# Performance work log

Measured on AMD Instinct MI355X. Metric: run time of the kernel, lower is better.

The kernel has to match this reference:

```python
import jax, jax.numpy as jnp
import numpy as np

H = 64       # HIDDEN_DIM
NH = 2       # attention heads
HD = H // NH # head dim = 32
M = 8        # MEMORY_SLOTS
V = 64       # VOCAB_SIZE


def layer_norm(x, g, b):
    m = x.mean(-1, keepdims=True)
    v = ((x - m) ** 2).mean(-1, keepdims=True)
    return (x - m) / jnp.sqrt(v + 1e-5) * g + b


def mha(x, wi, bi, wo, bo):
    # torch nn.MultiheadAttention, batch_first, self-attention, avg head weights
    B, L, _ = x.shape
    qkv = x @ wi.T + bi                      # (B,L,3H)
    q, k, v = jnp.split(qkv, 3, axis=-1)
    q = q.reshape(B, L, NH, HD)
    k = k.reshape(B, L, NH, HD)
    v = v.reshape(B, L, NH, HD)
    s = jnp.einsum('bqhd,bkhd->bhqk', q, k) / jnp.sqrt(jnp.float32(HD))
    w = jax.nn.softmax(s, axis=-1)           # (B,NH,L,L)
    o = jnp.einsum('bhqk,bkhd->bqhd', w, v).reshape(B, L, H)
    return o @ wo.T + bo, w.mean(axis=1)     # averaged over heads


def ffn(x, w1, b1, w2, b2):
    return jax.nn.relu(x @ w1.T + b1) @ w2.T + b2


def setup_inputs() -> dict:
    key = jax.random.key(0)
    ks = iter(jax.random.split(key, 48))
    p = lambda shape: jax.random.normal(next(ks), shape, jnp.float32) * 0.02
    B, L = 16, 2048
    inp = {
        'seq': jax.random.randint(next(ks), (B, L), 0, V, jnp.int64 if jax.config.jax_enable_x64 else jnp.int32),
        'query': jax.random.randint(next(ks), (B,), 0, V, jnp.int32),
        'target': jax.random.randint(next(ks), (B,), 0, V, jnp.int32),
        'embed': p((V, H)),
        'a1_wi': p((3 * H, H)), 'a1_bi': p((3 * H,)), 'a1_wo': p((H, H)), 'a1_bo': p((H,)),
        'ff1_w1': p((2 * H, H)), 'ff1_b1': p((2 * H,)), 'ff1_w2': p((H, 2 * H)), 'ff1_b2': p((H,)),
        'ln1a_g': jnp.ones((H,)), 'ln1a_b': jnp.zeros((H,)),
        'ln1b_g': jnp.ones((H,)), 'ln1b_b': jnp.zeros((H,)),
        'a2_wi': p((3 * H, H)), 'a2_bi': p((3 * H,)), 'a2_wo': p((H, H)), 'a2_bo': p((H,)),
        'ff2_w1': p((2 * H, H)), 'ff2_b1': p((2 * H,)), 'ff2_w2': p((H, 2 * H)), 'ff2_b2': p((H,)),
        'ln2a_g': jnp.ones((H,)), 'ln2a_b': jnp.zeros((H,)),
        'ln2b_g': jnp.ones((H,)), 'ln2b_b': jnp.zeros((H,)),
        'rq_w': p((H, H)), 'rq_b': p((H,)),
        'ro_w': p((V, H)), 'ro_b': p((V,)),
        'qemb': p((V, H)),
    }
    return inp


def reference(seq, query, target, embed,
              a1_wi, a1_bi, a1_wo, a1_bo, ff1_w1, ff1_b1, ff1_w2, ff1_b2,
              ln1a_g, ln1a_b, ln1b_g, ln1b_b,
              a2_wi, a2_bi, a2_wo, a2_bo, ff2_w1, ff2_b1, ff2_w2, ff2_b2,
              ln2a_g, ln2a_b, ln2b_g, ln2b_b,
              rq_w, rq_b, ro_w, ro_b, qemb):
    # encoder
    h = embed[seq]                                        # (B,L,H)
    a1, _ = mha(h, a1_wi, a1_bi, a1_wo, a1_bo)
    h = layer_norm(h + a1, ln1a_g, ln1a_b)
    h = layer_norm(h + ffn(h, ff1_w1, ff1_b1, ff1_w2, ff1_b2), ln1b_g, ln1b_b)
    a2, attn_w = mha(h, a2_wi, a2_bi, a2_wo, a2_bo)       # attn_w: (B,L,L)
    h = layer_norm(h + a2, ln2a_g, ln2a_b)
    h = layer_norm(h + ffn(h, ff2_w1, ff2_b1, ff2_w2, ff2_b2), ln2b_g, ln2b_b)

    # slot selection (write_mode='attention'): per-key importance, top-k
    importance = attn_w.mean(axis=1)                      # (B,L)
    _, topk = jax.lax.top_k(importance, M)                # (B,M)
    mem = jnp.take_along_axis(h, topk[:, :, None], axis=1)  # (B,M,H)

    # memory reader
    q_h = qemb[query]                                     # (B,H)
    q = q_h @ rq_w.T + rq_b                               # (B,H)
    scores = (q[:, None, :] * mem).sum(-1) / jnp.sqrt(jnp.float32(H))  # (B,M)
    weights = jax.nn.softmax(scores, axis=-1)[:, :, None]
    read = (weights * mem).sum(1)                         # (B,H)
    logits = read @ ro_w.T + ro_b                         # (B,V)

    logp = jax.nn.log_softmax(logits, axis=-1)
    loss = -jnp.mean(logp[jnp.arange(logits.shape[0]), target])
    return loss, attn_w
```

## Files before the change

kernel.cpp:

```cpp
#include <hip/hip_runtime.h>
#include <hip/hip_bf16.h>


typedef unsigned short u16;
#define LQ 2048
#define BBATCH 16
#define QKB 262144

typedef __attribute__((ext_vector_type(8))) short bf16x8;
typedef __attribute__((ext_vector_type(4))) float f32x4;

__device__ __forceinline__ float bfu2f(u16 x){ return __uint_as_float(((unsigned)x) << 16); }
__device__ __forceinline__ u16 f2bu(float f){ return __bfloat16_as_ushort(__float2bfloat16(f)); }

__device__ __forceinline__ unsigned cvtpk(float lo, float hi){
  unsigned r;
  asm("v_cvt_pk_bf16_f32 %0, %1, %2" : "=v"(r) : "v"(lo), "v"(hi));
  return r;
}

__device__ __forceinline__ const u16* qk_rowp(const u16* qk_r15, const u16* qk_ws,
                                              int bz, int row){
  const u16* base = (bz < 15) ? (qk_r15 + (size_t)bz*QKB) : qk_ws;
  return base + (size_t)row*128;
}
__device__ __forceinline__ u16* qk_rowp_w(u16* qk_r15, u16* qk_ws, int bz, int row){
  u16* base = (bz < 15) ? (qk_r15 + (size_t)bz*QKB) : qk_ws;
  return base + (size_t)row*128;
}

__global__ __launch_bounds__(256) void k_embed(const int* __restrict__ seq,
                                               const float* __restrict__ emb,
                                               u16* __restrict__ h,
                                               float* __restrict__ imp0,
                                               float* __restrict__ out0){
  int i = blockIdx.x*256 + threadIdx.x;
  if (i < 32768) imp0[i] = 0.f;
  if (i == 0) out0[0] = 0.f;
  int tok = i >> 6, d = i & 63;
  int v = seq[tok] & 63;
  h[i] = f2bu(emb[(v << 6) + d]);
}

template<int MODE>
__global__ __launch_bounds__(256) void k_qkv(const u16* __restrict__ X,
                                             const float* __restrict__ W,
                                             const float* __restrict__ bias,
                                             u16* __restrict__ dqk0,
                                             u16* __restrict__ dqk_r15,
                                             u16* __restrict__ dqk_ws,
                                             u16* __restrict__ vg){
  __shared__ u16 WL[192*64];
  __shared__ unsigned YL32[64*97];
  __shared__ float BS[192];
  const int t = threadIdx.x;
  for (int e=t; e<12288; e+=256){
    int m = e>>6, k = e&63;
    WL[m*64 + (k ^ ((m&7)<<3))] = f2bu(W[e]);
  }
  if (t < 192) BS[t] = bias[t];
  __syncthreads();
  const int lane = t & 63, wv = t >> 6;
  const int n = lane & 15, gq = lane >> 4;
  const int tok0 = blockIdx.x*64;
  const int tl = wv*16 + n;
  bf16x8 xf0 = *(const bf16x8*)(X + (size_t)(tok0+tl)*64 + gq*8);
  bf16x8 xf1 = *(const bf16x8*)(X + (size_t)(tok0+tl)*64 + 32 + gq*8);
  const float qs = 0.17677669529663688f;
  #pragma unroll
  for (int ct=0; ct<12; ct++){
    f32x4 c;
    #pragma unroll
    for (int r=0;r<4;r++) c[r] = BS[ct*16 + gq*4 + r];
    bf16x8 wf0 = *(const bf16x8*)(WL + (ct*16+n)*64 + ((gq*8) ^ ((n&7)<<3)));
    bf16x8 wf1 = *(const bf16x8*)(WL + (ct*16+n)*64 + ((32+gq*8) ^ ((n&7)<<3)));
    c = __builtin_amdgcn_mfma_f32_16x16x32_bf16(wf0, xf0, c, 0, 0, 0);
    c = __builtin_amdgcn_mfma_f32_16x16x32_bf16(wf1, xf1, c, 0, 0, 0);
    if (ct < 4){ c[0]*=qs; c[1]*=qs; c[2]*=qs; c[3]*=qs; }
    YL32[tl*97 + ct*8 + gq*2]     = cvtpk(c[0], c[1]);
    YL32[tl*97 + ct*8 + gq*2 + 1] = cvtpk(c[2], c[3]);
  }
  __syncthreads();
  const int b = tok0 >> 11, rbase = tok0 & 2047;
  #pragma unroll
  for (int i=0;i<16;i++){
    int idx = i*256 + t;
    int rl = idx>>6, cc = idx&63;
    u16* row = (MODE==0) ? (dqk0 + (size_t)(tok0+rl)*128)
                         : qk_rowp_w(dqk_r15, dqk_ws, b, rbase+rl);
    ((unsigned*)row)[cc] = YL32[rl*97 + cc];
  }
  #pragma unroll
  for (int i=0;i<4;i++){
    int gid = i*256 + t;
    int grp = gid>>6, d = gid&63;
    int j0 = rbase + grp*4;
    unsigned lohi[2];
    #pragma unroll
    for (int p=0;p<2;p++){
      unsigned w0 = YL32[(grp*4 + 2*p)*97 + 64 + (d>>1)];
      unsigned w1 = YL32[(grp*4 + 2*p + 1)*97 + 64 + (d>>1)];
      u16 a  = (d&1) ? (u16)(w0>>16) : (u16)(w0 & 0xffffu);
      u16 bb = (d&1) ? (u16)(w1>>16) : (u16)(w1 & 0xffffu);
      lohi[p] = (unsigned)a | ((unsigned)bb << 16);
    }
    size_t A = ((size_t)((b*64 + (j0>>5))*4 + ((j0>>2)&3))*64 + d)*8 + ((j0>>4)&1)*4;
    *(uint2*)(vg + A) = make_uint2(lohi[0], lohi[1]);
  }
}

template<int MODE>
__global__ __launch_bounds__(256) void k_attn_ln(const u16* __restrict__ PQK,
    const u16* __restrict__ QKWS, const u16* __restrict__ VG,
    const float* __restrict__ wo, const float* __restrict__ bo,
    const float* __restrict__ g, const float* __restrict__ be,
    u16* __restrict__ h, float* __restrict__ lout){
  __shared__ float R[4096];
  __shared__ float ST[32*68];
  __shared__ float DN[2][32];
  __shared__ float CB[192];
  const int lin = blockIdx.x;
  const int nid = (lin & 7)*128 + (lin >> 3);
  const int qt = nid & 63, bz = nid >> 6;
  const int t = threadIdx.x;
  const int lane = t & 63, wv = t >> 6;
  const int n = lane & 15, gq = lane >> 4;
  const f32x4 FZ = {0.f, 0.f, 0.f, 0.f};

  for (int e=t; e<2048; e+=256) R[e] = 0.f;
  if (t < 64) DN[t>>5][t&31] = 0.f;
  __syncthreads();

  bf16x8 qf[2][2];
  #pragma unroll
  for (int qa=0; qa<2; qa++){
    const u16* qrow = (MODE==0) ? (PQK + (size_t)(bz*LQ + qt*32 + qa*16 + n)*128)
                                : qk_rowp(PQK, QKWS, bz, qt*32 + qa*16 + n);
    qf[qa][0] = *(const bf16x8*)(qrow + gq*8);
    qf[qa][1] = *(const bf16x8*)(qrow + 32 + gq*8);
  }
  f32x4 o[2][2][2];
  #pragma unroll
  for (int qa=0; qa<2; qa++)
    #pragma unroll
    for (int hh=0; hh<2; hh++)
      #pragma unroll
      for (int db=0; db<2; db++) o[qa][hh][db] = FZ;
  float dacc[2][2] = {{0.f,0.f},{0.f,0.f}};

  #pragma unroll 1
  for (int kt=wv*8; kt<wv*8+8; kt++){
    #pragma unroll
    for (int hh=0; hh<2; hh++){
      bf16x8 kf[4];
      #pragma unroll
      for (int jb=0; jb<4; jb++){
        const u16* kr = (MODE==0) ? (PQK + (size_t)(bz*LQ + kt*64 + jb*16 + n)*128)
                                  : qk_rowp(PQK, QKWS, bz, kt*64 + jb*16 + n);
        kf[jb] = *(const bf16x8*)(kr + 64 + hh*32 + gq*8);
      }
      unsigned pk[2][4][2];
      #pragma unroll
      for (int qa=0; qa<2; qa++){
        f32x4 ev[4];
        #pragma unroll
        for (int jb=0; jb<4; jb++)
          ev[jb] = __builtin_amdgcn_mfma_f32_16x16x32_bf16(kf[jb], qf[qa][hh], FZ, 0, 0, 0);
        float ds = 0.f;
        #pragma unroll
        for (int jb=0; jb<4; jb++){
          float e0 = __expf(ev[jb][0]), e1 = __expf(ev[jb][1]);
          float e2 = __expf(ev[jb][2]), e3 = __expf(ev[jb][3]);
          ds += (e0+e1) + (e2+e3);
          pk[qa][jb][0] = cvtpk(e0, e1);
          pk[qa][jb][1] = cvtpk(e2, e3);
        }
        dacc[qa][hh] += ds;
      }
      #pragma unroll
      for (int kb=0; kb<2; kb++){
        union { unsigned u[4]; bf16x8 v; } af[2];
        #pragma unroll
        for (int qa=0; qa<2; qa++){
          af[qa].u[0] = pk[qa][2*kb][0];   af[qa].u[1] = pk[qa][2*kb][1];
          af[qa].u[2] = pk[qa][2*kb+1][0]; af[qa].u[3] = pk[qa][2*kb+1][1];
        }
        #pragma unroll
        for (int db=0; db<2; db++){
          const int d = hh*32 + db*16 + n;
          const bf16x8 vf = *(const bf16x8*)(VG +
              ((size_t)((bz*64 + kt*2 + kb)*4 + gq)*64 + d)*8);
          #pragma unroll
          for (int qa=0; qa<2; qa++)
            o[qa][hh][db] = __builtin_amdgcn_mfma_f32_16x16x32_bf16(af[qa].v, vf, o[qa][hh][db], 0, 0, 0);
        }
      }
    }
  }
  #pragma unroll
  for (int qa=0; qa<2; qa++)
    #pragma unroll
    for (int hh=0; hh<2; hh++){
      float s = dacc[qa][hh];
      s += __shfl_xor(s, 16);
      s += __shfl_xor(s, 32);
      if (gq == 0) atomicAdd(&DN[hh][qa*16 + n], s);
    }
  #pragma unroll
  for (int qa=0; qa<2; qa++)
    #pragma unroll
    for (int hh=0; hh<2; hh++)
      #pragma unroll
      for (int db=0; db<2; db++)
        #pragma unroll
        for (int r=0; r<4; r++)
          atomicAdd(&R[(qa*16 + gq*4 + r)*64 + hh*32 + db*16 + n], o[qa][hh][db][r]);
  __syncthreads();
  if (lout && t < 64)
    lout[(size_t)(bz*2 + (t>>5))*LQ + qt*32 + (t&31)] = DN[t>>5][t&31];
  for (int e=t; e<2048; e+=256){
    int q = e >> 6, d = e & 63;
    ST[q*68 + d] = R[e] / DN[d>>5][q];
  }
  __syncthreads();
  for (int e2=t; e2<4096; e2+=256){ int k=e2>>6, mo=e2&63; R[e2] = wo[mo*64+k]; }
  if (t < 64)       CB[t] = bo[t];
  else if (t < 128) CB[t] = g[t-64];
  else if (t < 192) CB[t] = be[t-128];
  __syncthreads();
  for (int r=0; r<8; r++){
    int tl = wv*8 + r;
    size_t gtok = (size_t)(bz*LQ + qt*32 + tl);
    float acc = CB[lane];
    for (int k=0; k<64; k++) acc += ST[tl*68 + k] * R[k*64 + lane];
    float rr = acc + bfu2f(h[gtok*64 + lane]);
    float s = rr;
    #pragma unroll
    for (int ofs=32; ofs; ofs>>=1) s += __shfl_xor(s, ofs);
    float mean = s * (1.f/64.f);
    float dv = rr - mean;
    float vs = dv*dv;
    #pragma unroll
    for (int ofs=32; ofs; ofs>>=1) vs += __shfl_xor(vs, ofs);
    float rstd = 1.f/sqrtf(vs*(1.f/64.f) + 1e-5f);
    h[gtok*64 + lane] = f2bu(dv*rstd*CB[64+lane] + CB[128+lane]);
  }
}

__global__ __launch_bounds__(256) void k_ffn(u16* __restrict__ h,
    const float* __restrict__ w1, const float* __restrict__ b1,
    const float* __restrict__ w2, const float* __restrict__ b2,
    const float* __restrict__ g, const float* __restrict__ be){
  __shared__ u16 W1L[128*64];
  __shared__ u16 W2L[64*192];
  __shared__ u16 YL[64*64];
  __shared__ float B1[128], B2F[64], G[64], Bb[64];
  const int t = threadIdx.x;
  for (int e=t; e<8192; e+=256){
    int row = e>>6, col = e&63;
    W1L[row*64 + (col ^ ((row&7)<<3))] = f2bu(w1[e]);
  }
  for (int e=t; e<12288; e+=256){
    int o = e/192, rem = e%192, u = rem>>5, gs = rem&31, gq2 = gs>>3, s = gs&7;
    float val;
    if (u < 4) val = w2[o*128 + u*32 + ((s>>2)<<4) + gq2*4 + (s&3)];
    else { int d = ((u-4)<<5) + gq2*8 + s; val = (d==o) ? 1.f : 0.f; }
    W2L[o*192 + ((u*32+gs) ^ ((o&7)<<3))] = f2bu(val);
  }
  if (t < 128) B1[t] = b1[t];
  if (t < 64){ B2F[t] = b2[t]; G[t] = g[t]; Bb[t] = be[t]; }
  __syncthreads();
  const int lane = t & 63, wv = t >> 6;
  const int n = lane & 15, gq = lane >> 4;
  const int tok0 = blockIdx.x*64 + wv*16;
  bf16x8 xf[2];
  xf[0] = *(const bf16x8*)(h + (size_t)(tok0+n)*64 + gq*8);
  xf[1] = *(const bf16x8*)(h + (size_t)(tok0+n)*64 + 32 + gq*8);
  f32x4 acc1[8];
  #pragma unroll
  for (int ct=0; ct<8; ct++){
    f32x4 c;
    #pragma unroll
    for (int r=0;r<4;r++) c[r] = B1[ct*16 + gq*4 + r];
    bf16x8 w1f0 = *(const bf16x8*)(W1L + (ct*16+n)*64 + ((gq*8) ^ ((n&7)<<3)));
    bf16x8 w1f1 = *(const bf16x8*)(W1L + (ct*16+n)*64 + ((32+gq*8) ^ ((n&7)<<3)));
    c = __builtin_amdgcn_mfma_f32_16x16x32_bf16(w1f0, xf[0], c, 0, 0, 0);
    c = __builtin_amdgcn_mfma_f32_16x16x32_bf16(w1f1, xf[1], c, 0, 0, 0);
    acc1[ct] = c;
  }
  f32x4 acc2[4];
  #pragma unroll
  for (int ot=0; ot<4; ot++)
    #pragma unroll
    for (int r=0;r<4;r++) acc2[ot][r] = B2F[ot*16 + gq*4 + r];
  #pragma unroll
  for (int u=0; u<6; u++){
    union { unsigned uu[4]; bf16x8 v; } bfr;
    if (u < 4){
      #pragma unroll
      for (int i=0;i<4;i++){
        int ct = u*2 + (i>>1);
        float a = fmaxf(acc1[ct][(2*i)&3], 0.f);
        float b = fmaxf(acc1[ct][(2*i+1)&3], 0.f);
        bfr.uu[i] = (unsigned)f2bu(a) | ((unsigned)f2bu(b) << 16);
      }
    } else {
      bfr.v = xf[u-4];
    }
    #pragma unroll
    for (int ot=0; ot<4; ot++){
      bf16x8 w2f = *(const bf16x8*)(W2L + (ot*16+n)*192 + ((u*32+gq*8) ^ ((n&7)<<3)));
      acc2[ot] = __builtin_amdgcn_mfma_f32_16x16x32_bf16(w2f, bfr.v, acc2[ot], 0, 0, 0);
    }
  }
  float s1 = 0.f;
  #pragma unroll
  for (int ot=0;ot<4;ot++)
    #pragma unroll
    for (int r=0;r<4;r++) s1 += acc2[ot][r];
  s1 += __shfl_xor(s1, 16); s1 += __shfl_xor(s1, 32);
  float mean = s1 * (1.f/64.f);
  float s2 = 0.f;
  #pragma unroll
  for (int ot=0;ot<4;ot++)
    #pragma unroll
    for (int r=0;r<4;r++){ float dv = acc2[ot][r]-mean; s2 += dv*dv; }
  s2 += __shfl_xor(s2, 16); s2 += __shfl_xor(s2, 32);
  float rstd = 1.f/sqrtf(s2*(1.f/64.f) + 1e-5f);
  #pragma unroll
  for (int ot=0;ot<4;ot++)
    #pragma unroll
    for (int r=0;r<4;r++){
      int o = ot*16 + gq*4 + r;
      float yv = (acc2[ot][r]-mean)*rstd*G[o] + Bb[o];
      YL[(wv*16+n)*64 + (o ^ ((n&7)<<3))] = f2bu(yv);
    }
  __syncthreads();
  unsigned* h32 = (unsigned*)(h + (size_t)(blockIdx.x)*64*64);
  #pragma unroll
  for (int i=0;i<8;i++){
    int idx = i*64 + lane;
    int row = wv*16 + (idx>>5), c32 = idx&31;
    unsigned vv = *(const unsigned*)(YL + row*64 + ((c32*2) ^ ((row&7)<<3)));
    h32[row*32 + c32] = vv;
  }
}

__global__ __launch_bounds__(256) void k_imp(const u16* __restrict__ qk_r15,
    const u16* __restrict__ qk_ws, const float* __restrict__ l2,
    float* __restrict__ imp, int bz0){
  __shared__ float IMPS[256];
  __shared__ float INVL[128];
  const int t = threadIdx.x;
  const int qt = blockIdx.x >> 3, ks = blockIdx.x & 7;
  const int bz = bz0;
  const int lane = t & 63, wv = t >> 6;
  const int n = lane & 15, gq = lane >> 4;
  const f32x4 FZ = {0.f, 0.f, 0.f, 0.f};
  if (t < 128) INVL[t] = 1.f / l2[(size_t)(bz*2 + (t>>6))*LQ + qt*64 + (t&63)];
  IMPS[t] = 0.f;
  bf16x8 qf0, qf1;
  {
    const u16* qrow = qk_rowp(qk_r15, qk_ws, bz, qt*64 + wv*16 + n);
    qf0 = *(const bf16x8*)(qrow + gq*8);
    qf1 = *(const bf16x8*)(qrow + 32 + gq*8);
  }
  __syncthreads();
  float iv0[4], iv1[4];
  #pragma unroll
  for (int r=0;r<4;r++){
    iv0[r] = INVL[wv*16 + gq*4 + r];
    iv1[r] = INVL[64 + wv*16 + gq*4 + r];
  }
  for (int kt=ks*4; kt<ks*4+4; kt++){
    #pragma unroll
    for (int jb=0; jb<4; jb++){
      const u16* kr = qk_rowp(qk_r15, qk_ws, bz, kt*64 + jb*16 + n);
      bf16x8 kf0 = *(const bf16x8*)(kr + 64 + gq*8);
      bf16x8 kf1 = *(const bf16x8*)(kr + 96 + gq*8);
      f32x4 e0 = __builtin_amdgcn_mfma_f32_16x16x32_bf16(qf0, kf0, FZ, 0, 0, 0);
      f32x4 e1 = __builtin_amdgcn_mfma_f32_16x16x32_bf16(qf1, kf1, FZ, 0, 0, 0);
      float cs = 0.f;
      #pragma unroll
      for (int r=0;r<4;r++)
        cs += 0.5f*(__expf(e0[r])*iv0[r] + __expf(e1[r])*iv1[r]);
      cs += __shfl_xor(cs, 16);
      cs += __shfl_xor(cs, 32);
      if (gq == 0) atomicAdd(&IMPS[(kt-ks*4)*64 + jb*16 + n], cs);
    }
  }
  __syncthreads();
  atomicAdd(&imp[bz*LQ + ks*256 + t], IMPS[t]);
}

template<int DOIMP>
__global__ __launch_bounds__(256) void k_pass2(const u16* __restrict__ qk_r15,
    const u16* __restrict__ qk_ws, const float* __restrict__ l2,
    float* __restrict__ part, float* __restrict__ wout, int bz0, int nper){
  __shared__ float STG[64*68];
  __shared__ float INVL[128];
  __shared__ float PIMP[256];
  const int x = blockIdx.x;
  const int nid = (x & 7)*nper + (x >> 3);
  const int bz = bz0 + (nid >> 8);
  const int rem = nid & 255;
  const int qt = rem >> 3, ks = rem & 7;
  const int t = threadIdx.x;
  const int lane = t & 63, wv = t >> 6;
  const int n = lane & 15, gq = lane >> 4;
  const f32x4 FZ = {0.f, 0.f, 0.f, 0.f};
  if (t < 128) INVL[t] = 1.f / l2[(size_t)(bz*2 + (t>>6))*LQ + qt*64 + (t&63)];
  if (DOIMP) PIMP[t] = 0.f;
  bf16x8 qf0, qf1;
  {
    const u16* qrow = qk_rowp(qk_r15, qk_ws, bz, qt*64 + wv*16 + n);
    qf0 = *(const bf16x8*)(qrow + gq*8);
    qf1 = *(const bf16x8*)(qrow + 32 + gq*8);
  }
  __syncthreads();
  const float iv0 = INVL[wv*16 + n], iv1 = INVL[64 + wv*16 + n];
  for (int kt = ks*4; kt < ks*4 + 4; kt++){
    #pragma unroll
    for (int jb=0; jb<4; jb++){
      const u16* kr = qk_rowp(qk_r15, qk_ws, bz, kt*64 + jb*16 + n);
      bf16x8 kf0 = *(const bf16x8*)(kr + 64 + gq*8);
      bf16x8 kf1 = *(const bf16x8*)(kr + 96 + gq*8);
      f32x4 e0 = __builtin_amdgcn_mfma_f32_16x16x32_bf16(kf0, qf0, FZ, 0, 0, 0);
      f32x4 e1 = __builtin_amdgcn_mfma_f32_16x16x32_bf16(kf1, qf1, FZ, 0, 0, 0);
      float4 w4;
      w4.x = 0.5f*(__expf(e0[0])*iv0 + __expf(e1[0])*iv1);
      w4.y = 0.5f*(__expf(e0[1])*iv0 + __expf(e1[1])*iv1);
      w4.z = 0.5f*(__expf(e0[2])*iv0 + __expf(e1[2])*iv1);
      w4.w = 0.5f*(__expf(e0[3])*iv0 + __expf(e1[3])*iv1);
      *(float4*)(&STG[(wv*16 + n)*68 + jb*16 + 4*gq]) = w4;
    }
    size_t base = 1 + (size_t)bz*LQ*LQ + (size_t)(qt*64)*LQ + (size_t)kt*64;
    float p = 0.f;
    for (int r=0; r<16; r++){
      int q = wv*16 + r;
      float v = STG[q*68 + lane];
      __builtin_nontemporal_store(v, &wout[base + (size_t)q*LQ + lane]);
      p += v;
    }
    if (DOIMP) atomicAdd(&PIMP[(kt-ks*4)*64 + lane], p);
  }
  if (DOIMP){
    __syncthreads();
    part[((size_t)qt*16 + bz)*LQ + ks*256 + t] = PIMP[t];
  }
}

__global__ __launch_bounds__(256) void k_reduce(const float* __restrict__ part,
                                                float* __restrict__ imp){
  int i = blockIdx.x*256 + threadIdx.x;
  int b = i >> 11, col = i & 2047;
  float s = 0.f;
  #pragma unroll 8
  for (int qt=0; qt<32; qt++) s += part[((size_t)qt*16 + b)*LQ + col];
  imp[b*LQ + col] = s;
}

__global__ __launch_bounds__(64) void k_select(const float* __restrict__ imp,
    const u16* __restrict__ h,
    const int* __restrict__ query, const int* __restrict__ target,
    const float* __restrict__ qemb, const float* __restrict__ rq_w, const float* __restrict__ rq_b,
    const float* __restrict__ ro_w, const float* __restrict__ ro_b, float* __restrict__ out0){
  __shared__ float v[2048];
  __shared__ float bv[64];
  __shared__ int   bi[64];
  __shared__ int   chosen;
  __shared__ int   topi[8];
  const int b = blockIdx.x, lane = threadIdx.x;
  for (int i=lane; i<2048; i+=64) v[i] = imp[b*2048 + i];
  __syncthreads();
  for (int m=0; m<8; m++){
    float best = -1e30f; int besti = 1<<30;
    for (int i=lane; i<2048; i+=64)
      if (v[i] > best || (v[i] == best && i < besti)){ best = v[i]; besti = i; }
    bv[lane] = best; bi[lane] = besti;
    __syncthreads();
    if (lane == 0){
      float B = bv[0]; int I = bi[0];
      for (int i2=1; i2<64; i2++)
        if (bv[i2] > B || (bv[i2] == B && bi[i2] < I)){ B = bv[i2]; I = bi[i2]; }
      int c = (I < 0) ? 0 : (I > 2047 ? 2047 : I);
      topi[m] = c;
      chosen = c;
    }
    __syncthreads();
    if (lane == 0) v[chosen] = -1e30f;
    __syncthreads();
  }
  float mv[8];
  #pragma unroll
  for (int m=0; m<8; m++){
    int idx = topi[m] & 2047;
    mv[m] = bfu2f(h[(size_t)(b*LQ + idx)*64 + lane]);
  }
  float qh = qemb[((query[b]&63)<<6) + lane];
  float qd = rq_b[lane];
  for (int k=0;k<64;k++) qd += __shfl(qh,k) * rq_w[lane*64 + k];
  float sc[8];
  #pragma unroll
  for (int m=0;m<8;m++){
    float p = qd * mv[m];
    #pragma unroll
    for (int o=32;o;o>>=1) p += __shfl_xor(p,o);
    sc[m] = p * 0.125f;
  }
  float mx = sc[0];
  #pragma unroll
  for (int m=1;m<8;m++) mx = fmaxf(mx, sc[m]);
  float den = 0.f, rd = 0.f;
  #pragma unroll
  for (int m=0;m<8;m++){ float w = __expf(sc[m]-mx); den += w; rd += w*mv[m]; }
  rd /= den;
  float lg = ro_b[lane];
  for (int d=0;d<64;d++) lg += __shfl(rd,d) * ro_w[lane*64 + d];
  float lmx = lg;
  #pragma unroll
  for (int o=32;o;o>>=1) lmx = fmaxf(lmx, __shfl_xor(lmx,o));
  float ex = __expf(lg - lmx), es = ex;
  #pragma unroll
  for (int o=32;o;o>>=1) es += __shfl_xor(es,o);
  float lt = __shfl(lg, target[b]&63);
  if (lane == 0) atomicAdd(out0, -(lt - lmx - logf(es)) * (1.f/16.f));
}

extern "C" void kernel_launch(void* const* d_in, const int* in_sizes, int n_in,
                              void* d_out, int out_size, void* d_ws, size_t ws_size,
                              hipStream_t stream){
  const int*   seq    = (const int*)  d_in[0];
  const int*   query  = (const int*)  d_in[1];
  const int*   target = (const int*)  d_in[2];
  const float* embed  = (const float*)d_in[3];
  const float* a1_wi  = (const float*)d_in[4];
  const float* a1_bi  = (const float*)d_in[5];
  const float* a1_wo  = (const float*)d_in[6];
  const float* a1_bo  = (const float*)d_in[7];
  const float* ff1_w1 = (const float*)d_in[8];
  const float* ff1_b1 = (const float*)d_in[9];
  const float* ff1_w2 = (const float*)d_in[10];
  const float* ff1_b2 = (const float*)d_in[11];
  const float* ln1a_g = (const float*)d_in[12];
  const float* ln1a_b = (const float*)d_in[13];
  const float* ln1b_g = (const float*)d_in[14];
  const float* ln1b_b = (const float*)d_in[15];
  const float* a2_wi  = (const float*)d_in[16];
  const float* a2_bi  = (const float*)d_in[17];
  const float* a2_wo  = (const float*)d_in[18];
  const float* a2_bo  = (const float*)d_in[19];
  const float* ff2_w1 = (const float*)d_in[20];
  const float* ff2_b1 = (const float*)d_in[21];
  const float* ff2_w2 = (const float*)d_in[22];
  const float* ff2_b2 = (const float*)d_in[23];
  const float* ln2a_g = (const float*)d_in[24];
  const float* ln2a_b = (const float*)d_in[25];
  const float* ln2b_g = (const float*)d_in[26];
  const float* ln2b_b = (const float*)d_in[27];
  const float* rq_w   = (const float*)d_in[28];
  const float* rq_b   = (const float*)d_in[29];
  const float* ro_w   = (const float*)d_in[30];
  const float* ro_b   = (const float*)d_in[31];
  const float* qemb   = (const float*)d_in[32];

  char* wsb      = (char*)d_ws;
  u16*  qk_ws    = (u16*)(wsb);
  float* ws_imp  = (float*)(wsb + 524288);
  float* ws_l    = (float*)(wsb + 655360);

  float* out_f  = (float*)d_out;
  u16* qk1     = (u16*)((char*)d_out + 4194368);
  u16* vg1     = (u16*)((char*)d_out + 12582976);
  u16* vg2     = (u16*)((char*)d_out + 4194368);
  u16* qk_r15  = (u16*)((char*)d_out + 251658304);
  u16* h16     = (u16*)((char*)d_out + 259522624);
  float* Ppart = (float*)((char*)d_out + 263716928);

  k_embed<<<8192,256,0,stream>>>(seq, embed, h16, ws_imp, out_f);
  k_qkv<0><<<512,256,0,stream>>>(h16, a1_wi, a1_bi, qk1, nullptr, nullptr, vg1);
  k_attn_ln<0><<<1024,256,0,stream>>>(qk1, nullptr, vg1,
                                      a1_wo, a1_bo, ln1a_g, ln1a_b, h16, nullptr);
  k_ffn<<<512,256,0,stream>>>(h16, ff1_w1, ff1_b1, ff1_w2, ff1_b2, ln1b_g, ln1b_b);
  k_qkv<1><<<512,256,0,stream>>>(h16, a2_wi, a2_bi, nullptr, qk_r15, qk_ws, vg2);
  k_attn_ln<1><<<1024,256,0,stream>>>(qk_r15, qk_ws, vg2,
                                      a2_wo, a2_bo, ln2a_g, ln2a_b, h16, ws_l);
  k_ffn<<<512,256,0,stream>>>(h16, ff2_w1, ff2_b1, ff2_w2, ff2_b2, ln2b_g, ln2b_b);
  k_pass2<1><<<3840,256,0,stream>>>(qk_r15, qk_ws, ws_l, Ppart, out_f, 0, 480);
  k_reduce<<<120,256,0,stream>>>(Ppart, ws_imp);
  k_imp<<<256,256,0,stream>>>(qk_r15, qk_ws, ws_l, ws_imp, 15);
  k_select<<<16,64,0,stream>>>(ws_imp, h16, query, target, qemb,
                               rq_w, rq_b, ro_w, ro_b, out_f);
  k_pass2<0><<<256,256,0,stream>>>(qk_r15, qk_ws, ws_l, nullptr, out_f, 15, 32);
}
```

Before: 802.6 us.

## Fuse embed into QKV, imp into pass2, reduce into select

Moves the embedding gather into the first QKV kernel, which now also writes h and zeroes the batch-15 importance buffer. The batch-15 importance blocks become extra blocks of the pass2 launch, and the partial-sum reduction moves into the select kernel. The top-k reduction now uses wave shuffles instead of shared-memory syncs. This drops three kernel launches and their intermediate global traffic, but only batch 15's importance is zeroed now, so the batch 0-14 slots of ws_imp go unused.

```diff
diff --git a/kernel.cpp b/kernel.cpp
--- a/kernel.cpp
+++ b/kernel.cpp
@@ -29,31 +29,28 @@
   return base + (size_t)row*128;
 }
 
-__global__ __launch_bounds__(256) void k_embed(const int* __restrict__ seq,
-                                               const float* __restrict__ emb,
-                                               u16* __restrict__ h,
-                                               float* __restrict__ imp0,
-                                               float* __restrict__ out0){
-  int i = blockIdx.x*256 + threadIdx.x;
-  if (i < 32768) imp0[i] = 0.f;
-  if (i == 0) out0[0] = 0.f;
-  int tok = i >> 6, d = i & 63;
-  int v = seq[tok] & 63;
-  h[i] = f2bu(emb[(v << 6) + d]);
-}
-
 template<int MODE>
 __global__ __launch_bounds__(256) void k_qkv(const u16* __restrict__ X,
+                                             const int* __restrict__ seq,
+                                             const float* __restrict__ emb,
                                              const float* __restrict__ W,
                                              const float* __restrict__ bias,
                                              u16* __restrict__ dqk0,
                                              u16* __restrict__ dqk_r15,
                                              u16* __restrict__ dqk_ws,
-                                             u16* __restrict__ vg){
+                                             u16* __restrict__ vg,
+                                             u16* __restrict__ hw,
+                                             float* __restrict__ imp15,
+                                             float* __restrict__ out0){
   __shared__ u16 WL[192*64];
   __shared__ unsigned YL32[64*97];
   __shared__ float BS[192];
   const int t = threadIdx.x;
+  if (MODE==0 && blockIdx.x==0){
+    #pragma unroll
+    for (int i=0;i<8;i++) imp15[i*256 + t] = 0.f;
+    if (t==0) out0[0] = 0.f;
+  }
   for (int e=t; e<12288; e+=256){
     int m = e>>6, k = e&63;
     WL[m*64 + (k ^ ((m&7)<<3))] = f2bu(W[e]);
@@ -64,8 +61,26 @@
   const int n = lane & 15, gq = lane >> 4;
   const int tok0 = blockIdx.x*64;
   const int tl = wv*16 + n;
-  bf16x8 xf0 = *(const bf16x8*)(X + (size_t)(tok0+tl)*64 + gq*8);
-  bf16x8 xf1 = *(const bf16x8*)(X + (size_t)(tok0+tl)*64 + 32 + gq*8);
+  bf16x8 xf0, xf1;
+  if (MODE==0){
+    int vv = seq[tok0+tl] & 63;
+    const float* er = emb + (vv << 6);
+    float4 p0 = *(const float4*)(er + gq*8);
+    float4 p1 = *(const float4*)(er + gq*8 + 4);
+    float4 p2 = *(const float4*)(er + 32 + gq*8);
+    float4 p3 = *(const float4*)(er + 32 + gq*8 + 4);
+    union { unsigned u[4]; bf16x8 v; } u0, u1;
+    u0.u[0]=cvtpk(p0.x,p0.y); u0.u[1]=cvtpk(p0.z,p0.w);
+    u0.u[2]=cvtpk(p1.x,p1.y); u0.u[3]=cvtpk(p1.z,p1.w);
+    u1.u[0]=cvtpk(p2.x,p2.y); u1.u[1]=cvtpk(p2.z,p2.w);
+    u1.u[2]=cvtpk(p3.x,p3.y); u1.u[3]=cvtpk(p3.z,p3.w);
+    xf0 = u0.v; xf1 = u1.v;
+    *(bf16x8*)(hw + (size_t)(tok0+tl)*64 + gq*8)      = xf0;
+    *(bf16x8*)(hw + (size_t)(tok0+tl)*64 + 32 + gq*8) = xf1;
+  } else {
+    xf0 = *(const bf16x8*)(X + (size_t)(tok0+tl)*64 + gq*8);
+    xf1 = *(const bf16x8*)(X + (size_t)(tok0+tl)*64 + 32 + gq*8);
+  }
   const float qs = 0.17677669529663688f;
   #pragma unroll
   for (int ct=0; ct<12; ct++){
@@ -346,69 +361,64 @@
   }
 }
 
-__global__ __launch_bounds__(256) void k_imp(const u16* __restrict__ qk_r15,
-    const u16* __restrict__ qk_ws, const float* __restrict__ l2,
-    float* __restrict__ imp, int bz0){
-  __shared__ float IMPS[256];
-  __shared__ float INVL[128];
-  const int t = threadIdx.x;
-  const int qt = blockIdx.x >> 3, ks = blockIdx.x & 7;
-  const int bz = bz0;
-  const int lane = t & 63, wv = t >> 6;
-  const int n = lane & 15, gq = lane >> 4;
-  const f32x4 FZ = {0.f, 0.f, 0.f, 0.f};
-  if (t < 128) INVL[t] = 1.f / l2[(size_t)(bz*2 + (t>>6))*LQ + qt*64 + (t&63)];
-  IMPS[t] = 0.f;
-  bf16x8 qf0, qf1;
-  {
-    const u16* qrow = qk_rowp(qk_r15, qk_ws, bz, qt*64 + wv*16 + n);
-    qf0 = *(const bf16x8*)(qrow + gq*8);
-    qf1 = *(const bf16x8*)(qrow + 32 + gq*8);
-  }
-  __syncthreads();
-  float iv0[4], iv1[4];
-  #pragma unroll
-  for (int r=0;r<4;r++){
-    iv0[r] = INVL[wv*16 + gq*4 + r];
-    iv1[r] = INVL[64 + wv*16 + gq*4 + r];
-  }
-  for (int kt=ks*4; kt<ks*4+4; kt++){
-    #pragma unroll
-    for (int jb=0; jb<4; jb++){
-      const u16* kr = qk_rowp(qk_r15, qk_ws, bz, kt*64 + jb*16 + n);
-      bf16x8 kf0 = *(const bf16x8*)(kr + 64 + gq*8);
-      bf16x8 kf1 = *(const bf16x8*)(kr + 96 + gq*8);
-      f32x4 e0 = __builtin_amdgcn_mfma_f32_16x16x32_bf16(qf0, kf0, FZ, 0, 0, 0);
-      f32x4 e1 = __builtin_amdgcn_mfma_f32_16x16x32_bf16(qf1, kf1, FZ, 0, 0, 0);
-      float cs = 0.f;
-      #pragma unroll
-      for (int r=0;r<4;r++)
-        cs += 0.5f*(__expf(e0[r])*iv0[r] + __expf(e1[r])*iv1[r]);
-      cs += __shfl_xor(cs, 16);
-      cs += __shfl_xor(cs, 32);
-      if (gq == 0) atomicAdd(&IMPS[(kt-ks*4)*64 + jb*16 + n], cs);
-    }
-  }
-  __syncthreads();
-  atomicAdd(&imp[bz*LQ + ks*256 + t], IMPS[t]);
-}
-
 template<int DOIMP>
 __global__ __launch_bounds__(256) void k_pass2(const u16* __restrict__ qk_r15,
     const u16* __restrict__ qk_ws, const float* __restrict__ l2,
-    float* __restrict__ part, float* __restrict__ wout, int bz0, int nper){
+    float* __restrict__ part, float* __restrict__ wout,
+    float* __restrict__ imp15, int bz0, int nper){
   __shared__ float STG[64*68];
   __shared__ float INVL[128];
   __shared__ float PIMP[256];
   const int x = blockIdx.x;
   const int nid = (x & 7)*nper + (x >> 3);
-  const int bz = bz0 + (nid >> 8);
-  const int rem = nid & 255;
-  const int qt = rem >> 3, ks = rem & 7;
   const int t = threadIdx.x;
   const int lane = t & 63, wv = t >> 6;
   const int n = lane & 15, gq = lane >> 4;
   const f32x4 FZ = {0.f, 0.f, 0.f, 0.f};
+
+  if (DOIMP && nid >= 3840){
+    const int idx = nid - 3840;
+    const int qt = idx >> 3, ks = idx & 7;
+    if (t < 128) INVL[t] = 1.f / l2[(size_t)(15*2 + (t>>6))*LQ + qt*64 + (t&63)];
+    PIMP[t] = 0.f;
+    bf16x8 qf0, qf1;
+    {
+      const u16* qrow = qk_rowp(qk_r15, qk_ws, 15, qt*64 + wv*16 + n);
+      qf0 = *(const bf16x8*)(qrow + gq*8);
+      qf1 = *(const bf16x8*)(qrow + 32 + gq*8);
+    }
+    __syncthreads();
+    float iv0[4], iv1[4];
+    #pragma unroll
+    for (int r=0;r<4;r++){
+      iv0[r] = INVL[wv*16 + gq*4 + r];
+      iv1[r] = INVL[64 + wv*16 + gq*4 + r];
+    }
+    for (int kt=ks*4; kt<ks*4+4; kt++){
+      #pragma unroll
+      for (int jb=0; jb<4; jb++){
+        const u16* kr = qk_rowp(qk_r15, qk_ws, 15, kt*64 + jb*16 + n);
+        bf16x8 kf0 = *(const bf16x8*)(kr + 64 + gq*8);
+        bf16x8 kf1 = *(const bf16x8*)(kr + 96 + gq*8);
+        f32x4 e0 = __builtin_amdgcn_mfma_f32_16x16x32_bf16(qf0, kf0, FZ, 0, 0, 0);
+        f32x4 e1 = __builtin_amdgcn_mfma_f32_16x16x32_bf16(qf1, kf1, FZ, 0, 0, 0);
+        float cs = 0.f;
+        #pragma unroll
+        for (int r=0;r<4;r++)
+          cs += 0.5f*(__expf(e0[r])*iv0[r] + __expf(e1[r])*iv1[r]);
+        cs += __shfl_xor(cs, 16);
+        cs += __shfl_xor(cs, 32);
+        if (gq == 0) atomicAdd(&PIMP[(kt-ks*4)*64 + jb*16 + n], cs);
+      }
+    }
+    __syncthreads();
+    atomicAdd(&imp15[ks*256 + t], PIMP[t]);
+    return;
+  }
+
+  const int bz = bz0 + (nid >> 8);
+  const int rem = nid & 255;
+  const int qt = rem >> 3, ks = rem & 7;
   if (t < 128) INVL[t] = 1.f / l2[(size_t)(bz*2 + (t>>6))*LQ + qt*64 + (t&63)];
   if (DOIMP) PIMP[t] = 0.f;
   bf16x8 qf0, qf1;
@@ -450,46 +460,40 @@
   }
 }
 
-__global__ __launch_bounds__(256) void k_reduce(const float* __restrict__ part,
-                                                float* __restrict__ imp){
-  int i = blockIdx.x*256 + threadIdx.x;
-  int b = i >> 11, col = i & 2047;
-  float s = 0.f;
-  #pragma unroll 8
-  for (int qt=0; qt<32; qt++) s += part[((size_t)qt*16 + b)*LQ + col];
-  imp[b*LQ + col] = s;
-}
-
-__global__ __launch_bounds__(64) void k_select(const float* __restrict__ imp,
-    const u16* __restrict__ h,
+__global__ __launch_bounds__(256) void k_select(const float* __restrict__ part,
+    const float* __restrict__ imp15, const u16* __restrict__ h,
     const int* __restrict__ query, const int* __restrict__ target,
     const float* __restrict__ qemb, const float* __restrict__ rq_w, const float* __restrict__ rq_b,
     const float* __restrict__ ro_w, const float* __restrict__ ro_b, float* __restrict__ out0){
   __shared__ float v[2048];
-  __shared__ float bv[64];
-  __shared__ int   bi[64];
-  __shared__ int   chosen;
-  __shared__ int   topi[8];
-  const int b = blockIdx.x, lane = threadIdx.x;
-  for (int i=lane; i<2048; i+=64) v[i] = imp[b*2048 + i];
-  __syncthreads();
+  const int b = blockIdx.x, t = threadIdx.x;
+  if (b < 15){
+    for (int c=t; c<2048; c+=256){
+      float s = 0.f;
+      #pragma unroll 8
+      for (int qt=0; qt<32; qt++) s += part[((size_t)qt*16 + b)*LQ + c];
+      v[c] = s;
+    }
+  } else {
+    for (int c=t; c<2048; c+=256) v[c] = imp15[c];
+  }
+  __syncthreads();
+  if (t >= 64) return;
+  const int lane = t;
+  int topi[8];
   for (int m=0; m<8; m++){
     float best = -1e30f; int besti = 1<<30;
     for (int i=lane; i<2048; i+=64)
       if (v[i] > best || (v[i] == best && i < besti)){ best = v[i]; besti = i; }
-    bv[lane] = best; bi[lane] = besti;
-    __syncthreads();
-    if (lane == 0){
-      float B = bv[0]; int I = bi[0];
-      for (int i2=1; i2<64; i2++)
-        if (bv[i2] > B || (bv[i2] == B && bi[i2] < I)){ B = bv[i2]; I = bi[i2]; }
-      int c = (I < 0) ? 0 : (I > 2047 ? 2047 : I);
-      topi[m] = c;
-      chosen = c;
-    }
-    __syncthreads();
-    if (lane == 0) v[chosen] = -1e30f;
-    __syncthreads();
+    #pragma unroll
+    for (int off=32; off; off>>=1){
+      float ob = __shfl_xor(best, off);
+      int   oi = __shfl_xor(besti, off);
+      if (ob > best || (ob == best && oi < besti)){ best = ob; besti = oi; }
+    }
+    int c = (besti < 0) ? 0 : (besti > 2047 ? 2047 : besti);
+    topi[m] = c;
+    v[c] = -1e30f;
   }
   float mv[8];
   #pragma unroll
@@ -568,6 +572,7 @@
   u16*  qk_ws    = (u16*)(wsb);
   float* ws_imp  = (float*)(wsb + 524288);
   float* ws_l    = (float*)(wsb + 655360);
+  float* imp15   = ws_imp + 15*LQ;
 
   float* out_f  = (float*)d_out;
   u16* qk1     = (u16*)((char*)d_out + 4194368);
@@ -577,19 +582,18 @@
   u16* h16     = (u16*)((char*)d_out + 259522624);
   float* Ppart = (float*)((char*)d_out + 263716928);
 
-  k_embed<<<8192,256,0,stream>>>(seq, embed, h16, ws_imp, out_f);
-  k_qkv<0><<<512,256,0,stream>>>(h16, a1_wi, a1_bi, qk1, nullptr, nullptr, vg1);
+  k_qkv<0><<<512,256,0,stream>>>(nullptr, seq, embed, a1_wi, a1_bi,
+                                 qk1, nullptr, nullptr, vg1, h16, imp15, out_f);
   k_attn_ln<0><<<1024,256,0,stream>>>(qk1, nullptr, vg1,
                                       a1_wo, a1_bo, ln1a_g, ln1a_b, h16, nullptr);
   k_ffn<<<512,256,0,stream>>>(h16, ff1_w1, ff1_b1, ff1_w2, ff1_b2, ln1b_g, ln1b_b);
-  k_qkv<1><<<512,256,0,stream>>>(h16, a2_wi, a2_bi, nullptr, qk_r15, qk_ws, vg2);
+  k_qkv<1><<<512,256,0,stream>>>(h16, nullptr, nullptr, a2_wi, a2_bi,
+                                 nullptr, qk_r15, qk_ws, vg2, nullptr, nullptr, nullptr);
   k_attn_ln<1><<<1024,256,0,stream>>>(qk_r15, qk_ws, vg2,
                                       a2_wo, a2_bo, ln2a_g, ln2a_b, h16, ws_l);
   k_ffn<<<512,256,0,stream>>>(h16, ff2_w1, ff2_b1, ff2_w2, ff2_b2, ln2b_g, ln2b_b);
-  k_pass2<1><<<3840,256,0,stream>>>(qk_r15, qk_ws, ws_l, Ppart, out_f, 0, 480);
-  k_reduce<<<120,256,0,stream>>>(Ppart, ws_imp);
-  k_imp<<<256,256,0,stream>>>(qk_r15, qk_ws, ws_l, ws_imp, 15);
-  k_select<<<16,64,0,stream>>>(ws_imp, h16, query, target, qemb,
-                               rq_w, rq_b, ro_w, ro_b, out_f);
-  k_pass2<0><<<256,256,0,stream>>>(qk_r15, qk_ws, ws_l, nullptr, out_f, 15, 32);
-}
+  k_pass2<1><<<4096,256,0,stream>>>(qk_r15, qk_ws, ws_l, Ppart, out_f, imp15, 0, 512);
+  k_select<<<16,256,0,stream>>>(Ppart, imp15, h16, query, target, qemb,
+                                rq_w, rq_b, ro_w, ro_b, out_f);
+  k_pass2<0><<<256,256,0,stream>>>(qk_r15, qk_ws, ws_l, nullptr, out_f, nullptr, 15, 32);
+}
```

After: 760.3 us (median of 2 runs). 1.06x faster.
